# Optimization experiments

Measured on AMD Instinct MI355X. Metric: run time of the kernel, lower is better.

Reference implementation:

```python
import jax, jax.numpy as jnp
import numpy as np


def setup_inputs() -> dict:
    key = jax.random.key(0)
    k1, k2 = jax.random.split(key)
    B, S, D, E = 4, 4096, 2048, 64
    x = jax.random.normal(k1, (B, S, D), dtype=jnp.float32)
    gate_w = jax.random.normal(k2, (E, D), dtype=jnp.float32) * (1.0 / np.sqrt(D))
    return {"x": x, "gate_w": gate_w, "top_k": 2}


def reference(x, gate_w, top_k):
    # logits = x @ W^T : [B, S, E]
    logits = jnp.einsum("bsd,ed->bse", x, gate_w)
    probs = jax.nn.softmax(logits, axis=-1)
    top_k_probs, top_k_indices = jax.lax.top_k(probs, top_k)
    top_k_probs = top_k_probs / jnp.sum(top_k_probs, axis=-1, keepdims=True)
    return (top_k_probs, top_k_indices, probs)
```

## Files before the change

### kernel.cpp

```cpp
#include <hip/hip_runtime.h>
#include <math.h>


typedef _Float16 half8  __attribute__((ext_vector_type(8)));
typedef float    floatx4 __attribute__((ext_vector_type(4)));

#define NTOK 16384
#define DDIM 2048
#define NE   64
#define NSTEP 32

__global__ __launch_bounds__(256) void w_split(const float* __restrict__ W,
                                               _Float16* __restrict__ whi,
                                               _Float16* __restrict__ wlo) {
    const int g = (blockIdx.x * 256 + threadIdx.x) * 8;
    const float4 v0 = *(const float4*)(W + g);
    const float4 v1 = *(const float4*)(W + g + 4);
    float f[8] = {v0.x, v0.y, v0.z, v0.w, v1.x, v1.y, v1.z, v1.w};
    half8 hi, lo;
#pragma unroll
    for (int j = 0; j < 8; ++j) {
        const _Float16 h = (_Float16)f[j];
        hi[j] = h;
        lo[j] = (_Float16)(f[j] - (float)h);
    }
    *(half8*)(whi + g) = hi;
    *(half8*)(wlo + g) = lo;
}

__global__ __launch_bounds__(256) void router_mfma(
    const float* __restrict__ x,
    const _Float16* __restrict__ whi,
    const _Float16* __restrict__ wlo,
    float* __restrict__ out)
{
    __shared__ float ex[2 * 64 * 20];
    __shared__ float lg[32 * 68];

    const int tid = threadIdx.x;
    const int L   = tid & 63;
    const int wv  = __builtin_amdgcn_readfirstlane(tid >> 6);
    const int eh  = wv & 1;
    const int kh  = wv >> 1;
    const int c   = L & 15;
    const int q   = L >> 4;
    const int tok0 = blockIdx.x * 32;

    const float*    ax0 = x   + (size_t)(tok0 + c) * DDIM + kh * 1024 + q * 8;
    const float*    ax1 = ax0 + 16 * DDIM;
    const _Float16* b0h = whi + (size_t)(eh * 32 + c) * DDIM + kh * 1024 + q * 8;
    const _Float16* b1h = b0h + 16 * DDIM;
    const _Float16* b0l = wlo + (size_t)(eh * 32 + c) * DDIM + kh * 1024 + q * 8;
    const _Float16* b1l = b0l + 16 * DDIM;

    float4 pa[2][2][2];
    pa[0][0][0] = *(const float4*)(ax0);
    pa[0][0][1] = *(const float4*)(ax0 + 4);
    pa[0][1][0] = *(const float4*)(ax1);
    pa[0][1][1] = *(const float4*)(ax1 + 4);

    floatx4 acc[2][2];
#pragma unroll
    for (int i = 0; i < 2; ++i)
#pragma unroll
        for (int j = 0; j < 2; ++j) acc[i][j] = (floatx4)0.f;

#pragma unroll 2
    for (int s = 0; s < NSTEP; ++s) {
        const int cur = s & 1, nxt = cur ^ 1;
        const int o = s * 32;

        half8 bh0 = *(const half8*)(b0h + o);
        half8 bh1 = *(const half8*)(b1h + o);
        half8 bl0 = *(const half8*)(b0l + o);
        half8 bl1 = *(const half8*)(b1l + o);

        if (s + 1 < NSTEP) {
            const int on = o + 32;
            pa[nxt][0][0] = *(const float4*)(ax0 + on);
            pa[nxt][0][1] = *(const float4*)(ax0 + on + 4);
            pa[nxt][1][0] = *(const float4*)(ax1 + on);
            pa[nxt][1][1] = *(const float4*)(ax1 + on + 4);
        }

        half8 ah[2], al[2];
#pragma unroll
        for (int mt = 0; mt < 2; ++mt) {
            const float4 u = pa[cur][mt][0];
            const float4 v = pa[cur][mt][1];
            float f[8] = {u.x, u.y, u.z, u.w, v.x, v.y, v.z, v.w};
#pragma unroll
            for (int j = 0; j < 8; ++j) {
                const _Float16 h = (_Float16)f[j];
                ah[mt][j] = h;
                al[mt][j] = (_Float16)(f[j] - (float)h);
            }
        }

#pragma unroll
        for (int mt = 0; mt < 2; ++mt) {
            acc[mt][0] = __builtin_amdgcn_mfma_f32_16x16x32_f16(ah[mt], bh0, acc[mt][0], 0, 0, 0);
            acc[mt][0] = __builtin_amdgcn_mfma_f32_16x16x32_f16(al[mt], bh0, acc[mt][0], 0, 0, 0);
            acc[mt][0] = __builtin_amdgcn_mfma_f32_16x16x32_f16(ah[mt], bl0, acc[mt][0], 0, 0, 0);
            acc[mt][1] = __builtin_amdgcn_mfma_f32_16x16x32_f16(ah[mt], bh1, acc[mt][1], 0, 0, 0);
            acc[mt][1] = __builtin_amdgcn_mfma_f32_16x16x32_f16(al[mt], bh1, acc[mt][1], 0, 0, 0);
            acc[mt][1] = __builtin_amdgcn_mfma_f32_16x16x32_f16(ah[mt], bl1, acc[mt][1], 0, 0, 0);
        }
    }

    if (kh == 1) {
        float* p = &ex[(eh * 64 + L) * 20];
        *(float4*)(p + 0)  = make_float4(acc[0][0][0], acc[0][0][1], acc[0][0][2], acc[0][0][3]);
        *(float4*)(p + 4)  = make_float4(acc[0][1][0], acc[0][1][1], acc[0][1][2], acc[0][1][3]);
        *(float4*)(p + 8)  = make_float4(acc[1][0][0], acc[1][0][1], acc[1][0][2], acc[1][0][3]);
        *(float4*)(p + 12) = make_float4(acc[1][1][0], acc[1][1][1], acc[1][1][2], acc[1][1][3]);
    }
    __syncthreads();
    if (kh == 0) {
        const float* p = &ex[(eh * 64 + L) * 20];
        float4 t;
        t = *(const float4*)(p + 0);  acc[0][0][0] += t.x; acc[0][0][1] += t.y; acc[0][0][2] += t.z; acc[0][0][3] += t.w;
        t = *(const float4*)(p + 4);  acc[0][1][0] += t.x; acc[0][1][1] += t.y; acc[0][1][2] += t.z; acc[0][1][3] += t.w;
        t = *(const float4*)(p + 8);  acc[1][0][0] += t.x; acc[1][0][1] += t.y; acc[1][0][2] += t.z; acc[1][0][3] += t.w;
        t = *(const float4*)(p + 12); acc[1][1][0] += t.x; acc[1][1][1] += t.y; acc[1][1][2] += t.z; acc[1][1][3] += t.w;
#pragma unroll
        for (int mt = 0; mt < 2; ++mt)
#pragma unroll
            for (int nt = 0; nt < 2; ++nt)
#pragma unroll
                for (int r = 0; r < 4; ++r)
                    lg[(mt * 16 + q * 4 + r) * 68 + eh * 32 + nt * 16 + c] = acc[mt][nt][r];
    }
    __syncthreads();

    if (tid < 32) {
        const int token = tok0 + tid;
        float* row = &lg[tid * 68];
        float p[NE];
#pragma unroll
        for (int e = 0; e < NE; ++e) p[e] = row[e];

        float m = p[0];
#pragma unroll
        for (int e = 1; e < NE; ++e) m = fmaxf(m, p[e]);
        float s = 0.f;
#pragma unroll
        for (int e = 0; e < NE; ++e) { p[e] = expf(p[e] - m); s += p[e]; }
        const float inv = 1.f / s;

        float v1 = -1.f; int i1 = 0;
#pragma unroll
        for (int e = 0; e < NE; ++e) { if (p[e] > v1) { v1 = p[e]; i1 = e; } }
        float v2 = -1.f; int i2 = 0;
#pragma unroll
        for (int e = 0; e < NE; ++e) { if (e != i1 && p[e] > v2) { v2 = p[e]; i2 = e; } }

        const float ts = v1 + v2;
        float* out_tp = out;
        float* out_ti = out + 2 * NTOK;
        *(float2*)(out_tp + token * 2) = make_float2(v1 / ts, v2 / ts);
        *(float2*)(out_ti + token * 2) = make_float2((float)i1, (float)i2);

#pragma unroll
        for (int e = 0; e < NE; ++e) row[e] = p[e] * inv;
    }
    __syncthreads();

    {
        float* out_p = out + 4 * NTOK + (size_t)tok0 * NE;
#pragma unroll
        for (int i = 0; i < 2; ++i) {
            const int f  = tid + 256 * i;
            const int r  = f >> 4, c4 = f & 15;
            const float4 v = *(const float4*)&lg[r * 68 + 4 * c4];
            *(float4*)(out_p + f * 4) = v;
        }
    }
}

extern "C" void kernel_launch(void* const* d_in, const int* in_sizes, int n_in,
                              void* d_out, int out_size, void* d_ws, size_t ws_size,
                              hipStream_t stream) {
    const float* x = (const float*)d_in[0];
    const float* W = (const float*)d_in[1];
    float* out     = (float*)d_out;
    _Float16* whi  = (_Float16*)d_ws;
    _Float16* wlo  = whi + (size_t)NE * DDIM;

    w_split<<<dim3(64), dim3(256), 0, stream>>>(W, whi, wlo);
    router_mfma<<<dim3(NTOK / 32), dim3(256), 0, stream>>>(x, whi, wlo, out);
}
```

Before: 219.4 us.

## Split K into four quarters with 512-thread blocks and prefetch weights

Each block now runs 8 waves instead of 4. The K dimension is split into four 512-wide quarters instead of two halves, so each wave's loop is half as long, and the partial sums are reduced through a larger shared-memory buffer. The fp16 hi/lo weight loads are also double-buffered alongside the x prefetch, which hides their latency. The goal is more memory-level parallelism per CU for this bandwidth-bound GEMV-like pass over x, at the cost of more registers, more LDS use and a larger cross-wave reduction.

```diff
diff --git a/kernel.cpp b/kernel.cpp
--- a/kernel.cpp
+++ b/kernel.cpp
@@ -8,7 +8,7 @@
 #define NTOK 16384
 #define DDIM 2048
 #define NE   64
-#define NSTEP 32
+#define NSTEP 16
 
 __global__ __launch_bounds__(256) void w_split(const float* __restrict__ W,
                                                _Float16* __restrict__ whi,
@@ -28,36 +28,43 @@
     *(half8*)(wlo + g) = lo;
 }
 
-__global__ __launch_bounds__(256) void router_mfma(
+__global__ __launch_bounds__(512) void router_mfma(
     const float* __restrict__ x,
     const _Float16* __restrict__ whi,
     const _Float16* __restrict__ wlo,
     float* __restrict__ out)
 {
-    __shared__ float ex[2 * 64 * 20];
+    __shared__ float ex[3 * 2 * 64 * 20];
     __shared__ float lg[32 * 68];
 
     const int tid = threadIdx.x;
     const int L   = tid & 63;
     const int wv  = __builtin_amdgcn_readfirstlane(tid >> 6);
     const int eh  = wv & 1;
-    const int kh  = wv >> 1;
+    const int kq  = wv >> 1;
     const int c   = L & 15;
     const int q   = L >> 4;
     const int tok0 = blockIdx.x * 32;
+    const int kb   = kq * 512;
 
-    const float*    ax0 = x   + (size_t)(tok0 + c) * DDIM + kh * 1024 + q * 8;
+    const float*    ax0 = x   + (size_t)(tok0 + c) * DDIM + kb + q * 8;
     const float*    ax1 = ax0 + 16 * DDIM;
-    const _Float16* b0h = whi + (size_t)(eh * 32 + c) * DDIM + kh * 1024 + q * 8;
+    const _Float16* b0h = whi + (size_t)(eh * 32 + c) * DDIM + kb + q * 8;
     const _Float16* b1h = b0h + 16 * DDIM;
-    const _Float16* b0l = wlo + (size_t)(eh * 32 + c) * DDIM + kh * 1024 + q * 8;
+    const _Float16* b0l = wlo + (size_t)(eh * 32 + c) * DDIM + kb + q * 8;
     const _Float16* b1l = b0l + 16 * DDIM;
 
     float4 pa[2][2][2];
+    half8  pbh[2][2], pbl[2][2];
+
     pa[0][0][0] = *(const float4*)(ax0);
     pa[0][0][1] = *(const float4*)(ax0 + 4);
     pa[0][1][0] = *(const float4*)(ax1);
     pa[0][1][1] = *(const float4*)(ax1 + 4);
+    pbh[0][0] = *(const half8*)(b0h);
+    pbh[0][1] = *(const half8*)(b1h);
+    pbl[0][0] = *(const half8*)(b0l);
+    pbl[0][1] = *(const half8*)(b1l);
 
     floatx4 acc[2][2];
 #pragma unroll
@@ -68,19 +75,17 @@
 #pragma unroll 2
     for (int s = 0; s < NSTEP; ++s) {
         const int cur = s & 1, nxt = cur ^ 1;
-        const int o = s * 32;
-
-        half8 bh0 = *(const half8*)(b0h + o);
-        half8 bh1 = *(const half8*)(b1h + o);
-        half8 bl0 = *(const half8*)(b0l + o);
-        half8 bl1 = *(const half8*)(b1l + o);
 
         if (s + 1 < NSTEP) {
-            const int on = o + 32;
+            const int on = (s + 1) * 32;
             pa[nxt][0][0] = *(const float4*)(ax0 + on);
             pa[nxt][0][1] = *(const float4*)(ax0 + on + 4);
             pa[nxt][1][0] = *(const float4*)(ax1 + on);
             pa[nxt][1][1] = *(const float4*)(ax1 + on + 4);
+            pbh[nxt][0] = *(const half8*)(b0h + on);
+            pbh[nxt][1] = *(const half8*)(b1h + on);
+            pbl[nxt][0] = *(const half8*)(b0l + on);
+            pbl[nxt][1] = *(const half8*)(b1l + on);
         }
 
         half8 ah[2], al[2];
@@ -99,30 +104,33 @@
 
 #pragma unroll
         for (int mt = 0; mt < 2; ++mt) {
-            acc[mt][0] = __builtin_amdgcn_mfma_f32_16x16x32_f16(ah[mt], bh0, acc[mt][0], 0, 0, 0);
-            acc[mt][0] = __builtin_amdgcn_mfma_f32_16x16x32_f16(al[mt], bh0, acc[mt][0], 0, 0, 0);
-            acc[mt][0] = __builtin_amdgcn_mfma_f32_16x16x32_f16(ah[mt], bl0, acc[mt][0], 0, 0, 0);
-            acc[mt][1] = __builtin_amdgcn_mfma_f32_16x16x32_f16(ah[mt], bh1, acc[mt][1], 0, 0, 0);
-            acc[mt][1] = __builtin_amdgcn_mfma_f32_16x16x32_f16(al[mt], bh1, acc[mt][1], 0, 0, 0);
-            acc[mt][1] = __builtin_amdgcn_mfma_f32_16x16x32_f16(ah[mt], bl1, acc[mt][1], 0, 0, 0);
+            acc[mt][0] = __builtin_amdgcn_mfma_f32_16x16x32_f16(ah[mt], pbh[cur][0], acc[mt][0], 0, 0, 0);
+            acc[mt][0] = __builtin_amdgcn_mfma_f32_16x16x32_f16(al[mt], pbh[cur][0], acc[mt][0], 0, 0, 0);
+            acc[mt][0] = __builtin_amdgcn_mfma_f32_16x16x32_f16(ah[mt], pbl[cur][0], acc[mt][0], 0, 0, 0);
+            acc[mt][1] = __builtin_amdgcn_mfma_f32_16x16x32_f16(ah[mt], pbh[cur][1], acc[mt][1], 0, 0, 0);
+            acc[mt][1] = __builtin_amdgcn_mfma_f32_16x16x32_f16(al[mt], pbh[cur][1], acc[mt][1], 0, 0, 0);
+            acc[mt][1] = __builtin_amdgcn_mfma_f32_16x16x32_f16(ah[mt], pbl[cur][1], acc[mt][1], 0, 0, 0);
         }
     }
 
-    if (kh == 1) {
-        float* p = &ex[(eh * 64 + L) * 20];
+    if (kq != 0) {
+        float* p = &ex[(((kq - 1) * 2 + eh) * 64 + L) * 20];
         *(float4*)(p + 0)  = make_float4(acc[0][0][0], acc[0][0][1], acc[0][0][2], acc[0][0][3]);
         *(float4*)(p + 4)  = make_float4(acc[0][1][0], acc[0][1][1], acc[0][1][2], acc[0][1][3]);
         *(float4*)(p + 8)  = make_float4(acc[1][0][0], acc[1][0][1], acc[1][0][2], acc[1][0][3]);
         *(float4*)(p + 12) = make_float4(acc[1][1][0], acc[1][1][1], acc[1][1][2], acc[1][1][3]);
     }
     __syncthreads();
-    if (kh == 0) {
-        const float* p = &ex[(eh * 64 + L) * 20];
-        float4 t;
-        t = *(const float4*)(p + 0);  acc[0][0][0] += t.x; acc[0][0][1] += t.y; acc[0][0][2] += t.z; acc[0][0][3] += t.w;
-        t = *(const float4*)(p + 4);  acc[0][1][0] += t.x; acc[0][1][1] += t.y; acc[0][1][2] += t.z; acc[0][1][3] += t.w;
-        t = *(const float4*)(p + 8);  acc[1][0][0] += t.x; acc[1][0][1] += t.y; acc[1][0][2] += t.z; acc[1][0][3] += t.w;
-        t = *(const float4*)(p + 12); acc[1][1][0] += t.x; acc[1][1][1] += t.y; acc[1][1][2] += t.z; acc[1][1][3] += t.w;
+    if (kq == 0) {
+#pragma unroll
+        for (int kk = 0; kk < 3; ++kk) {
+            const float* p = &ex[((kk * 2 + eh) * 64 + L) * 20];
+            float4 t;
+            t = *(const float4*)(p + 0);  acc[0][0][0] += t.x; acc[0][0][1] += t.y; acc[0][0][2] += t.z; acc[0][0][3] += t.w;
+            t = *(const float4*)(p + 4);  acc[0][1][0] += t.x; acc[0][1][1] += t.y; acc[0][1][2] += t.z; acc[0][1][3] += t.w;
+            t = *(const float4*)(p + 8);  acc[1][0][0] += t.x; acc[1][0][1] += t.y; acc[1][0][2] += t.z; acc[1][0][3] += t.w;
+            t = *(const float4*)(p + 12); acc[1][1][0] += t.x; acc[1][1][1] += t.y; acc[1][1][2] += t.z; acc[1][1][3] += t.w;
+        }
 #pragma unroll
         for (int mt = 0; mt < 2; ++mt)
 #pragma unroll
@@ -168,13 +176,10 @@
 
     {
         float* out_p = out + 4 * NTOK + (size_t)tok0 * NE;
-#pragma unroll
-        for (int i = 0; i < 2; ++i) {
-            const int f  = tid + 256 * i;
-            const int r  = f >> 4, c4 = f & 15;
-            const float4 v = *(const float4*)&lg[r * 68 + 4 * c4];
-            *(float4*)(out_p + f * 4) = v;
-        }
+        const int f  = tid;
+        const int r  = f >> 4, c4 = f & 15;
+        const float4 v = *(const float4*)&lg[r * 68 + 4 * c4];
+        *(float4*)(out_p + f * 4) = v;
     }
 }
 
@@ -188,5 +193,5 @@
     _Float16* wlo  = whi + (size_t)NE * DDIM;
 
     w_split<<<dim3(64), dim3(256), 0, stream>>>(W, whi, wlo);
-    router_mfma<<<dim3(NTOK / 32), dim3(256), 0, stream>>>(x, whi, wlo, out);
+    router_mfma<<<dim3(NTOK / 32), dim3(512), 0, stream>>>(x, whi, wlo, out);
 }
```

Result: slower. 225.1 us (+2.6%).

## Stage x and W tiles in swizzled LDS with double buffering, 64 tokens per block

Applied to the files above, without the earlier changes.

Each block now handles 64 tokens with 512 threads. Per K-step it cooperatively loads x and a pre-swizzled hi/lo fp16 W image into double-buffered LDS, splitting x into hi/lo once per element instead of once per wave. W is read once per block rather than separately per wave from global memory. A new w_split kernel writes W in a step-major, XOR-swizzled image to avoid LDS bank conflicts. The cost is a __syncthreads per step and a large LDS footprint (64KB of tiles), which may lower occupancy.

```diff
diff --git a/kernel.cpp b/kernel.cpp
--- a/kernel.cpp
+++ b/kernel.cpp
@@ -5,59 +5,83 @@
 typedef _Float16 half8  __attribute__((ext_vector_type(8)));
 typedef float    floatx4 __attribute__((ext_vector_type(4)));
 
-#define NTOK 16384
-#define DDIM 2048
-#define NE   64
+#define NTOK  16384
+#define DDIM  2048
+#define NE    64
+#define TPB   64
 #define NSTEP 32
 
-__global__ __launch_bounds__(256) void w_split(const float* __restrict__ W,
-                                               _Float16* __restrict__ whi,
-                                               _Float16* __restrict__ wlo) {
-    const int g = (blockIdx.x * 256 + threadIdx.x) * 8;
-    const float4 v0 = *(const float4*)(W + g);
-    const float4 v1 = *(const float4*)(W + g + 4);
-    float f[8] = {v0.x, v0.y, v0.z, v0.w, v1.x, v1.y, v1.z, v1.w};
-    half8 hi, lo;
+__device__ inline void split8(const float4& a, const float4& b,
+                              half8& hi, half8& lo) {
+    float f[8] = {a.x, a.y, a.z, a.w, b.x, b.y, b.z, b.w};
 #pragma unroll
     for (int j = 0; j < 8; ++j) {
         const _Float16 h = (_Float16)f[j];
         hi[j] = h;
         lo[j] = (_Float16)(f[j] - (float)h);
     }
-    *(half8*)(whi + g) = hi;
-    *(half8*)(wlo + g) = lo;
-}
-
-__global__ __launch_bounds__(256) void router_mfma(
+}
+
+__global__ __launch_bounds__(256) void w_split(const float* __restrict__ W,
+                                               _Float16* __restrict__ img) {
+    const int idx  = blockIdx.x * 256 + threadIdx.x;
+    const int step = idx >> 10;
+    const int u    = idx & 1023;
+    const int hl   = u >> 9;
+    const int v    = u & 511;
+    const int e    = v >> 3, g = v & 7;
+    const float* src = W + (size_t)e * DDIM + step * 64 + 8 * (g ^ (e & 7));
+    const float4 a = *(const float4*)(src);
+    const float4 b = *(const float4*)(src + 4);
+    half8 hi, lo;
+    split8(a, b, hi, lo);
+    *(half8*)(img + (size_t)idx * 8) = (hl == 0) ? hi : lo;
+}
+
+__global__ __launch_bounds__(512) void router_mfma(
     const float* __restrict__ x,
-    const _Float16* __restrict__ whi,
-    const _Float16* __restrict__ wlo,
+    const _Float16* __restrict__ img,
     float* __restrict__ out)
 {
-    __shared__ float ex[2 * 64 * 20];
-    __shared__ float lg[32 * 68];
+    __shared__ __align__(16) float tiles[16384];
+    __shared__ __align__(16) float lg[TPB * 68];
 
     const int tid = threadIdx.x;
     const int L   = tid & 63;
     const int wv  = __builtin_amdgcn_readfirstlane(tid >> 6);
-    const int eh  = wv & 1;
-    const int kh  = wv >> 1;
-    const int c   = L & 15;
-    const int q   = L >> 4;
-    const int tok0 = blockIdx.x * 32;
-
-    const float*    ax0 = x   + (size_t)(tok0 + c) * DDIM + kh * 1024 + q * 8;
-    const float*    ax1 = ax0 + 16 * DDIM;
-    const _Float16* b0h = whi + (size_t)(eh * 32 + c) * DDIM + kh * 1024 + q * 8;
-    const _Float16* b1h = b0h + 16 * DDIM;
-    const _Float16* b0l = wlo + (size_t)(eh * 32 + c) * DDIM + kh * 1024 + q * 8;
-    const _Float16* b1l = b0l + 16 * DDIM;
-
-    float4 pa[2][2][2];
-    pa[0][0][0] = *(const float4*)(ax0);
-    pa[0][0][1] = *(const float4*)(ax0 + 4);
-    pa[0][1][0] = *(const float4*)(ax1);
-    pa[0][1][1] = *(const float4*)(ax1 + 4);
+    const int kh  = wv & 1;
+    const int nh  = (wv >> 1) & 1;
+    const int mh  = wv >> 2;
+    const int c   = L & 15, q = L >> 4;
+    const int tok0 = blockIdx.x * TPB;
+
+    const int gfrag = (q + 4 * kh) ^ (L & 7);
+    int aoff[2], boff[2];
+#pragma unroll
+    for (int mt = 0; mt < 2; ++mt)
+        aoff[mt] = ((mh * 32 + mt * 16 + c) * 8 + gfrag) * 8;
+#pragma unroll
+    for (int nt = 0; nt < 2; ++nt)
+        boff[nt] = ((nh * 32 + nt * 16 + c) * 8 + gfrag) * 8;
+
+    const int sr = tid >> 3, so = tid & 7;
+    const float* xsrc = x + (size_t)(tok0 + sr) * DDIM + 8 * (so ^ (sr & 7));
+    const int    xdst = (sr * 8 + so) * 8;
+    const float* wsrc = (const float*)img;
+
+    {
+        const float4 xa  = *(const float4*)(xsrc);
+        const float4 xb  = *(const float4*)(xsrc + 4);
+        const float4 wh4 = *(const float4*)(wsrc + (size_t)tid * 4);
+        const float4 wl4 = *(const float4*)(wsrc + (size_t)(512 + tid) * 4);
+        _Float16* nb = (_Float16*)&tiles[0];
+        half8 hi, lo; split8(xa, xb, hi, lo);
+        *(half8*)(nb + xdst)        = hi;
+        *(half8*)(nb + 4096 + xdst) = lo;
+        *(float4*)(nb + 8192  + tid * 8) = wh4;
+        *(float4*)(nb + 12288 + tid * 8) = wl4;
+    }
+    __syncthreads();
 
     floatx4 acc[2][2];
 #pragma unroll
@@ -66,94 +90,100 @@
         for (int j = 0; j < 2; ++j) acc[i][j] = (floatx4)0.f;
 
 #pragma unroll 2
-    for (int s = 0; s < NSTEP; ++s) {
-        const int cur = s & 1, nxt = cur ^ 1;
-        const int o = s * 32;
-
-        half8 bh0 = *(const half8*)(b0h + o);
-        half8 bh1 = *(const half8*)(b1h + o);
-        half8 bl0 = *(const half8*)(b0l + o);
-        half8 bl1 = *(const half8*)(b1l + o);
-
-        if (s + 1 < NSTEP) {
-            const int on = o + 32;
-            pa[nxt][0][0] = *(const float4*)(ax0 + on);
-            pa[nxt][0][1] = *(const float4*)(ax0 + on + 4);
-            pa[nxt][1][0] = *(const float4*)(ax1 + on);
-            pa[nxt][1][1] = *(const float4*)(ax1 + on + 4);
-        }
-
-        half8 ah[2], al[2];
+    for (int t = 0; t < NSTEP; ++t) {
+        float4 xa, xb, wh4, wl4;
+        if (t + 1 < NSTEP) {
+            xa  = *(const float4*)(xsrc + (t + 1) * 64);
+            xb  = *(const float4*)(xsrc + (t + 1) * 64 + 4);
+            wh4 = *(const float4*)(wsrc + (size_t)((t + 1) * 1024 + tid) * 4);
+            wl4 = *(const float4*)(wsrc + (size_t)((t + 1) * 1024 + 512 + tid) * 4);
+        }
+
+        const _Float16* base = (const _Float16*)&tiles[(t & 1) * 8192];
+        const _Float16* xh = base;
+        const _Float16* xl = base + 4096;
+        const _Float16* wh = base + 8192;
+        const _Float16* wl = base + 12288;
+
+        half8 Ah[2], Al[2], Bh[2], Bl[2];
 #pragma unroll
         for (int mt = 0; mt < 2; ++mt) {
-            const float4 u = pa[cur][mt][0];
-            const float4 v = pa[cur][mt][1];
-            float f[8] = {u.x, u.y, u.z, u.w, v.x, v.y, v.z, v.w};
-#pragma unroll
-            for (int j = 0; j < 8; ++j) {
-                const _Float16 h = (_Float16)f[j];
-                ah[mt][j] = h;
-                al[mt][j] = (_Float16)(f[j] - (float)h);
+            Ah[mt] = *(const half8*)(xh + aoff[mt]);
+            Al[mt] = *(const half8*)(xl + aoff[mt]);
+        }
+#pragma unroll
+        for (int nt = 0; nt < 2; ++nt) {
+            Bh[nt] = *(const half8*)(wh + boff[nt]);
+            Bl[nt] = *(const half8*)(wl + boff[nt]);
+        }
+#pragma unroll
+        for (int mt = 0; mt < 2; ++mt)
+#pragma unroll
+            for (int nt = 0; nt < 2; ++nt) {
+                acc[mt][nt] = __builtin_amdgcn_mfma_f32_16x16x32_f16(Ah[mt], Bh[nt], acc[mt][nt], 0, 0, 0);
+                acc[mt][nt] = __builtin_amdgcn_mfma_f32_16x16x32_f16(Al[mt], Bh[nt], acc[mt][nt], 0, 0, 0);
+                acc[mt][nt] = __builtin_amdgcn_mfma_f32_16x16x32_f16(Ah[mt], Bl[nt], acc[mt][nt], 0, 0, 0);
             }
-        }
-
-#pragma unroll
-        for (int mt = 0; mt < 2; ++mt) {
-            acc[mt][0] = __builtin_amdgcn_mfma_f32_16x16x32_f16(ah[mt], bh0, acc[mt][0], 0, 0, 0);
-            acc[mt][0] = __builtin_amdgcn_mfma_f32_16x16x32_f16(al[mt], bh0, acc[mt][0], 0, 0, 0);
-            acc[mt][0] = __builtin_amdgcn_mfma_f32_16x16x32_f16(ah[mt], bl0, acc[mt][0], 0, 0, 0);
-            acc[mt][1] = __builtin_amdgcn_mfma_f32_16x16x32_f16(ah[mt], bh1, acc[mt][1], 0, 0, 0);
-            acc[mt][1] = __builtin_amdgcn_mfma_f32_16x16x32_f16(al[mt], bh1, acc[mt][1], 0, 0, 0);
-            acc[mt][1] = __builtin_amdgcn_mfma_f32_16x16x32_f16(ah[mt], bl1, acc[mt][1], 0, 0, 0);
-        }
-    }
-
+
+        if (t + 1 < NSTEP) {
+            _Float16* nb = (_Float16*)&tiles[((t + 1) & 1) * 8192];
+            half8 hi, lo; split8(xa, xb, hi, lo);
+            *(half8*)(nb + xdst)        = hi;
+            *(half8*)(nb + 4096 + xdst) = lo;
+            *(float4*)(nb + 8192  + tid * 8) = wh4;
+            *(float4*)(nb + 12288 + tid * 8) = wl4;
+        }
+        __syncthreads();
+    }
+
+    float* exch = tiles;
+    const int p = wv >> 1;
     if (kh == 1) {
-        float* p = &ex[(eh * 64 + L) * 20];
-        *(float4*)(p + 0)  = make_float4(acc[0][0][0], acc[0][0][1], acc[0][0][2], acc[0][0][3]);
-        *(float4*)(p + 4)  = make_float4(acc[0][1][0], acc[0][1][1], acc[0][1][2], acc[0][1][3]);
-        *(float4*)(p + 8)  = make_float4(acc[1][0][0], acc[1][0][1], acc[1][0][2], acc[1][0][3]);
-        *(float4*)(p + 12) = make_float4(acc[1][1][0], acc[1][1][1], acc[1][1][2], acc[1][1][3]);
+        float* e0 = &exch[(p * 64 + L) * 20];
+        *(float4*)(e0 + 0)  = make_float4(acc[0][0][0], acc[0][0][1], acc[0][0][2], acc[0][0][3]);
+        *(float4*)(e0 + 4)  = make_float4(acc[0][1][0], acc[0][1][1], acc[0][1][2], acc[0][1][3]);
+        *(float4*)(e0 + 8)  = make_float4(acc[1][0][0], acc[1][0][1], acc[1][0][2], acc[1][0][3]);
+        *(float4*)(e0 + 12) = make_float4(acc[1][1][0], acc[1][1][1], acc[1][1][2], acc[1][1][3]);
     }
     __syncthreads();
     if (kh == 0) {
-        const float* p = &ex[(eh * 64 + L) * 20];
-        float4 t;
-        t = *(const float4*)(p + 0);  acc[0][0][0] += t.x; acc[0][0][1] += t.y; acc[0][0][2] += t.z; acc[0][0][3] += t.w;
-        t = *(const float4*)(p + 4);  acc[0][1][0] += t.x; acc[0][1][1] += t.y; acc[0][1][2] += t.z; acc[0][1][3] += t.w;
-        t = *(const float4*)(p + 8);  acc[1][0][0] += t.x; acc[1][0][1] += t.y; acc[1][0][2] += t.z; acc[1][0][3] += t.w;
-        t = *(const float4*)(p + 12); acc[1][1][0] += t.x; acc[1][1][1] += t.y; acc[1][1][2] += t.z; acc[1][1][3] += t.w;
+        const float* e0 = &exch[(p * 64 + L) * 20];
+        float4 v;
+        v = *(const float4*)(e0 + 0);  acc[0][0][0] += v.x; acc[0][0][1] += v.y; acc[0][0][2] += v.z; acc[0][0][3] += v.w;
+        v = *(const float4*)(e0 + 4);  acc[0][1][0] += v.x; acc[0][1][1] += v.y; acc[0][1][2] += v.z; acc[0][1][3] += v.w;
+        v = *(const float4*)(e0 + 8);  acc[1][0][0] += v.x; acc[1][0][1] += v.y; acc[1][0][2] += v.z; acc[1][0][3] += v.w;
+        v = *(const float4*)(e0 + 12); acc[1][1][0] += v.x; acc[1][1][1] += v.y; acc[1][1][2] += v.z; acc[1][1][3] += v.w;
 #pragma unroll
         for (int mt = 0; mt < 2; ++mt)
 #pragma unroll
             for (int nt = 0; nt < 2; ++nt)
 #pragma unroll
                 for (int r = 0; r < 4; ++r)
-                    lg[(mt * 16 + q * 4 + r) * 68 + eh * 32 + nt * 16 + c] = acc[mt][nt][r];
-    }
-    __syncthreads();
-
-    if (tid < 32) {
+                    lg[(mh * 32 + mt * 16 + q * 4 + r) * 68 + nh * 32 + nt * 16 + c] = acc[mt][nt][r];
+    }
+    __syncthreads();
+
+    if (tid < 64) {
         const int token = tok0 + tid;
         float* row = &lg[tid * 68];
-        float p[NE];
-#pragma unroll
-        for (int e = 0; e < NE; ++e) p[e] = row[e];
-
-        float m = p[0];
-#pragma unroll
-        for (int e = 1; e < NE; ++e) m = fmaxf(m, p[e]);
+        float pr[NE];
+#pragma unroll
+        for (int e = 0; e < NE; ++e) pr[e] = row[e];
+
+        float m = pr[0];
+#pragma unroll
+        for (int e = 1; e < NE; ++e) m = fmaxf(m, pr[e]);
         float s = 0.f;
 #pragma unroll
-        for (int e = 0; e < NE; ++e) { p[e] = expf(p[e] - m); s += p[e]; }
+        for (int e = 0; e < NE; ++e) { pr[e] = expf(pr[e] - m); s += pr[e]; }
         const float inv = 1.f / s;
 
         float v1 = -1.f; int i1 = 0;
 #pragma unroll
-        for (int e = 0; e < NE; ++e) { if (p[e] > v1) { v1 = p[e]; i1 = e; } }
+        for (int e = 0; e < NE; ++e) { if (pr[e] > v1) { v1 = pr[e]; i1 = e; } }
         float v2 = -1.f; int i2 = 0;
 #pragma unroll
-        for (int e = 0; e < NE; ++e) { if (e != i1 && p[e] > v2) { v2 = p[e]; i2 = e; } }
+        for (int e = 0; e < NE; ++e) { if (e != i1 && pr[e] > v2) { v2 = pr[e]; i2 = e; } }
 
         const float ts = v1 + v2;
         float* out_tp = out;
@@ -162,7 +192,7 @@
         *(float2*)(out_ti + token * 2) = make_float2((float)i1, (float)i2);
 
 #pragma unroll
-        for (int e = 0; e < NE; ++e) row[e] = p[e] * inv;
+        for (int e = 0; e < NE; ++e) row[e] = pr[e] * inv;
     }
     __syncthreads();
 
@@ -170,8 +200,8 @@
         float* out_p = out + 4 * NTOK + (size_t)tok0 * NE;
 #pragma unroll
         for (int i = 0; i < 2; ++i) {
-            const int f  = tid + 256 * i;
-            const int r  = f >> 4, c4 = f & 15;
+            const int f = tid + 512 * i;
+            const int r = f >> 4, c4 = f & 15;
             const float4 v = *(const float4*)&lg[r * 68 + 4 * c4];
             *(float4*)(out_p + f * 4) = v;
         }
@@ -184,9 +214,8 @@
     const float* x = (const float*)d_in[0];
     const float* W = (const float*)d_in[1];
     float* out     = (float*)d_out;
-    _Float16* whi  = (_Float16*)d_ws;
-    _Float16* wlo  = whi + (size_t)NE * DDIM;
-
-    w_split<<<dim3(64), dim3(256), 0, stream>>>(W, whi, wlo);
-    router_mfma<<<dim3(NTOK / 32), dim3(256), 0, stream>>>(x, whi, wlo, out);
-}
+    _Float16* img  = (_Float16*)d_ws;
+
+    w_split<<<dim3(128), dim3(256), 0, stream>>>(W, img);
+    router_mfma<<<dim3(NTOK / TPB), dim3(512), 0, stream>>>(x, img, out);
+}
```

Result: faster. 212.0 us (-3.4%).
